# Optimization experiments

Hardware: AMD Instinct MI355X
Metric: run time of the kernel (lower is better)

Reference implementation:

```python
import jax, jax.numpy as jnp
import numpy as np
import math

H_SP, W_SP = 200, 200          # BEV spatial shape (single level, m == h)
D_MODEL = 256
N_HEADS = 8
N_POINTS = 4
D_HEAD = D_MODEL // N_HEADS


def _grid_init_bias():
    # Matches TemporalSelfAttention._reset_parameters for sampling_offsets.bias
    thetas = np.arange(N_HEADS, dtype=np.float32) * (2.0 * np.pi / N_HEADS)
    grid = np.stack([np.cos(thetas), np.sin(thetas)], -1)
    grid = grid / np.abs(grid).max(-1, keepdims=True)
    grid = np.tile(grid[:, None, None, :], (1, 1, N_POINTS, 1))  # (NH, 1, P, 2)
    for i in range(N_POINTS):
        grid[:, :, i, :] *= (i + 1)
    return jnp.asarray(grid.reshape(-1), dtype=jnp.float32)


def setup_inputs() -> dict:
    key = jax.random.key(0)
    ks = jax.random.split(key, 10)
    N = 1
    Lq = H_SP * W_SP
    Lin = H_SP * W_SP
    xav = math.sqrt(6.0 / (2 * D_MODEL))
    query = jax.random.normal(ks[0], (N, Lq, D_MODEL), jnp.float32)
    query_pos = jax.random.normal(ks[1], (N, Lq, D_MODEL), jnp.float32)
    reference_points = jax.random.uniform(ks[2], (N, Lq, 1, 2), jnp.float32)
    input_flatten = jax.random.normal(ks[3], (N, Lin, D_MODEL), jnp.float32)
    W_value = jax.random.uniform(ks[4], (D_MODEL, D_MODEL), jnp.float32, -xav, xav)
    b_value = jnp.zeros((D_MODEL,), jnp.float32)
    # small random weights (trained-model-like) + canonical grid bias
    W_off = jax.random.normal(ks[5], (N_HEADS * N_POINTS * 2, D_MODEL), jnp.float32) * 0.005
    b_off = _grid_init_bias()
    W_attn = jax.random.normal(ks[6], (N_HEADS * N_POINTS, D_MODEL), jnp.float32) * 0.02
    b_attn = jnp.zeros((N_HEADS * N_POINTS,), jnp.float32)
    W_out = jax.random.uniform(ks[7], (D_MODEL, D_MODEL), jnp.float32, -xav, xav)
    b_out = jnp.zeros((D_MODEL,), jnp.float32)
    return dict(query=query, query_pos=query_pos, reference_points=reference_points,
                input_flatten=input_flatten, W_value=W_value, b_value=b_value,
                W_off=W_off, b_off=b_off, W_attn=W_attn, b_attn=b_attn,
                W_out=W_out, b_out=b_out)


def _bilinear_sample(vflat, x, y):
    # vflat: (N, NH, H*W, DH); x, y: (N, NH, K) pixel coords (align_corners=False)
    # Zero padding outside the feature map, matching the MSDeformAttn CUDA kernel.
    x0f = jnp.floor(x)
    y0f = jnp.floor(y)
    x0 = x0f.astype(jnp.int32)
    y0 = y0f.astype(jnp.int32)
    lw = x - x0f
    lh = y - y0f
    gather = jax.vmap(jax.vmap(lambda v, i: v[i]))  # over batch, head
    acc = jnp.zeros(x.shape + (vflat.shape[-1],), vflat.dtype)
    corners = ((y0, x0, (1.0 - lh) * (1.0 - lw)),
               (y0, x0 + 1, (1.0 - lh) * lw),
               (y0 + 1, x0, lh * (1.0 - lw)),
               (y0 + 1, x0 + 1, lh * lw))
    for yi, xi, wgt in corners:
        valid = ((xi >= 0) & (xi < W_SP) & (yi >= 0) & (yi < H_SP)).astype(vflat.dtype)
        idx = jnp.clip(yi, 0, H_SP - 1) * W_SP + jnp.clip(xi, 0, W_SP - 1)
        g = gather(vflat, idx)                      # (N, NH, K, DH)
        acc = acc + (wgt * valid)[..., None] * g
    return acc


def reference(query, query_pos, reference_points, input_flatten,
              W_value, b_value, W_off, b_off, W_attn, b_attn, W_out, b_out):
    N, Lq, _ = query.shape
    q = query + query_pos
    value = input_flatten @ W_value.T + b_value                     # (N, Lin, D)
    value = value.reshape(N, -1, N_HEADS, D_HEAD).transpose(0, 2, 1, 3)  # (N, NH, Lin, DH)
    off = (q @ W_off.T + b_off).reshape(N, Lq, N_HEADS, N_POINTS, 2)
    attn = jax.nn.softmax((q @ W_attn.T + b_attn).reshape(N, Lq, N_HEADS, N_POINTS), axis=-1)
    norm = jnp.array([W_SP, H_SP], jnp.float32)                      # offset_normalizer (w, h)
    ref = reference_points[:, :, 0, :][:, :, None, None, :]          # (N, Lq, 1, 1, 2)
    loc = ref + off / norm                                           # (N, Lq, NH, P, 2) in [0,1]
    x = (loc[..., 0] * W_SP - 0.5).transpose(0, 2, 1, 3).reshape(N, N_HEADS, Lq * N_POINTS)
    y = (loc[..., 1] * H_SP - 0.5).transpose(0, 2, 1, 3).reshape(N, N_HEADS, Lq * N_POINTS)
    sampled = _bilinear_sample(value, x, y).reshape(N, N_HEADS, Lq, N_POINTS, D_HEAD)
    out = jnp.einsum('nhqpd,nqhp->nqhd', sampled, attn).reshape(N, Lq, D_MODEL)
    return out @ W_out.T + b_out
```

## Files before the change

### kernel.cpp

```cpp
#include <hip/hip_runtime.h>
#include <math.h>

#define LQ 40000
#define DMODEL 256
#define NHD 8
#define NPT 4
#define DHD 32
#define HSP 200
#define WSP 200

typedef short s16x8 __attribute__((ext_vector_type(8)));
typedef float f32x4 __attribute__((ext_vector_type(4)));

__device__ __forceinline__ unsigned short f2b(float f) {
    unsigned u = __builtin_bit_cast(unsigned, f);
    u += 0x7FFFu + ((u >> 16) & 1u);
    return (unsigned short)(u >> 16);
}
__device__ __forceinline__ float b2f(unsigned short u) {
    return __builtin_bit_cast(float, ((unsigned)u) << 16);
}
__device__ __forceinline__ void pk8(const float4& v0, const float4& v1,
                                    unsigned short* o) {
    o[0] = f2b(v0.x); o[1] = f2b(v0.y); o[2] = f2b(v0.z); o[3] = f2b(v0.w);
    o[4] = f2b(v1.x); o[5] = f2b(v1.y); o[6] = f2b(v1.z); o[7] = f2b(v1.w);
}


__global__ __launch_bounds__(256) void convert_weights(
    const float* __restrict__ Wv, const float* __restrict__ Woff,
    const float* __restrict__ Wattn, const float* __restrict__ Wout,
    unsigned short* __restrict__ dst)
{
    int u = blockIdx.x * 256 + threadIdx.x;
    int lane = u & 63, ks = (u >> 6) & 7, slot = u >> 9;
    int l15 = lane & 15, quad = lane >> 4;
    const float* src;
    if (slot < 16) {
        src = Wv + (size_t)(slot * 16 + l15) * 256;
    } else if (slot < 22) {
        int col = (slot - 16) * 16 + l15;
        src = (col < 64) ? Woff + (size_t)col * 256
                         : Wattn + (size_t)(col - 64) * 256;
    } else {
        src = Wout + (size_t)((slot - 22) * 16 + l15) * 256;
    }
    int k0 = ks * 32 + quad * 8;
    float4 v0 = *(const float4*)(src + k0);
    float4 v1 = *(const float4*)(src + k0 + 4);
    union { unsigned short u16[8]; uint4 v; } tmp;
    pk8(v0, v1, tmp.u16);
    *(uint4*)(dst + (size_t)u * 8) = tmp.v;
}

template <int NT, int TPW, int CMODE, bool HasA2>
__global__ __launch_bounds__(256, 2) void gemm_fused(
    const float* __restrict__ A, const float* __restrict__ A2,
    const unsigned short* __restrict__ Wf,
    const float* __restrict__ b1, const float* __restrict__ b2, int split,
    void* __restrict__ Cv)
{
    const int t = threadIdx.x;
    const int wave = t >> 6, lane = t & 63;
    const int l15 = lane & 15, quad = lane >> 4;

    s16x8 bf[TPW][8];
    float bias[TPW];
#pragma unroll
    for (int j = 0; j < TPW; ++j) {
        bias[j] = 0.f;
        int c = wave * TPW + j;
        if (c < NT) {
#pragma unroll
            for (int ks = 0; ks < 8; ++ks)
                bf[j][ks] = *(const s16x8*)&Wf[(size_t)(c * 8 + ks) * 512 + lane * 8];
            int col = c * 16 + l15;
            bias[j] = (col < split) ? b1[col] : b2[col - split];
        }
    }

#pragma unroll
    for (int s = 0; s < 2; ++s) {
        const size_t g = (size_t)blockIdx.x * 2 + s;
        const size_t rowoff = (g * 16 + l15) * 256;
        s16x8 a[8];
#pragma unroll
        for (int ks = 0; ks < 8; ++ks) {
            int k0 = ks * 32 + quad * 8;
            float4 v0 = *(const float4*)(A + rowoff + k0);
            float4 v1 = *(const float4*)(A + rowoff + k0 + 4);
            if constexpr (HasA2) {
                float4 w0 = *(const float4*)(A2 + rowoff + k0);
                float4 w1 = *(const float4*)(A2 + rowoff + k0 + 4);
                v0.x += w0.x; v0.y += w0.y; v0.z += w0.z; v0.w += w0.w;
                v1.x += w1.x; v1.y += w1.y; v1.z += w1.z; v1.w += w1.w;
            }
            union { unsigned short u16[8]; s16x8 v; } tmp;
            pk8(v0, v1, tmp.u16);
            a[ks] = tmp.v;
        }
#pragma unroll
        for (int j = 0; j < TPW; ++j) {
            int c = wave * TPW + j;
            if (c < NT) {
                f32x4 acc = (f32x4){0.f, 0.f, 0.f, 0.f};
#pragma unroll
                for (int ks = 0; ks < 8; ++ks)
                    acc = __builtin_amdgcn_mfma_f32_16x16x32_bf16(a[ks], bf[j][ks],
                                                                  acc, 0, 0, 0);
#pragma unroll
                for (int r2 = 0; r2 < 4; ++r2) {
                    size_t row = g * 16 + quad * 4 + r2;
                    float v = acc[r2] + bias[j];
                    if constexpr (CMODE == 1) {
                        ((unsigned short*)Cv)[(((size_t)(c >> 1) * LQ + row) << 5)
                                              + ((c & 1) << 4) + l15] = f2b(v);
                    } else if constexpr (CMODE == 2) {
                        int col = c * 16 + l15;
                        int hh, jj;
                        if (col < 64) { hh = col >> 3; jj = col & 7; }
                        else          { hh = (col - 64) >> 2; jj = 8 + (col & 3); }
                        ((float*)Cv)[((size_t)hh * LQ + row) * 12 + jj] = v;
                    } else {
                        ((float*)Cv)[row * (NT * 16) + c * 16 + l15] = v;
                    }
                }
            }
        }
    }
}

template <int NT, int TPW>
__global__ __launch_bounds__(256, 2) void gemm_rs(
    const unsigned short* __restrict__ Af, const unsigned short* __restrict__ Wf,
    const float* __restrict__ b1, float* __restrict__ C)
{
    const int t = threadIdx.x;
    const int wave = t >> 6, lane = t & 63;
    const int l15 = lane & 15, quad = lane >> 4;

    s16x8 bf[TPW][8];
    float bias[TPW];
#pragma unroll
    for (int j = 0; j < TPW; ++j) {
        int c = wave * TPW + j;
#pragma unroll
        for (int ks = 0; ks < 8; ++ks)
            bf[j][ks] = *(const s16x8*)&Wf[(size_t)(c * 8 + ks) * 512 + lane * 8];
        bias[j] = b1[c * 16 + l15];
    }

#pragma unroll
    for (int s = 0; s < 2; ++s) {
        const size_t g = (size_t)blockIdx.x * 2 + s;
        s16x8 a[8];
#pragma unroll
        for (int ks = 0; ks < 8; ++ks)
            a[ks] = *(const s16x8*)&Af[g * 4096 + ks * 512 + lane * 8];
#pragma unroll
        for (int j = 0; j < TPW; ++j) {
            int c = wave * TPW + j;
            f32x4 acc = (f32x4){0.f, 0.f, 0.f, 0.f};
#pragma unroll
            for (int ks = 0; ks < 8; ++ks)
                acc = __builtin_amdgcn_mfma_f32_16x16x32_bf16(a[ks], bf[j][ks],
                                                              acc, 0, 0, 0);
#pragma unroll
            for (int r2 = 0; r2 < 4; ++r2) {
                size_t row = g * 16 + quad * 4 + r2;
                C[row * (NT * 16) + c * 16 + l15] = acc[r2] + bias[j];
            }
        }
    }
}

__global__ __launch_bounds__(256) void sample_kernel(
    const float* __restrict__ raw2, const float* __restrict__ rp,
    const unsigned short* __restrict__ value, unsigned short* __restrict__ outa)
{
    __shared__ int4   sIdx[64][4];
    __shared__ float4 sW[64][4];

    const int h = blockIdx.x & 7;
    const int q0 = (blockIdx.x >> 3) * 64;
    const int t = threadIdx.x;
    {
        const int qi = t >> 2, p = t & 3;
        const int q = q0 + qi;
        const float* r = raw2 + ((size_t)h * LQ + q) * 12;
        float l0 = r[8], l1 = r[9], l2 = r[10], l3 = r[11];
        float mx = fmaxf(fmaxf(l0, l1), fmaxf(l2, l3));
        float e0 = __expf(l0 - mx), e1 = __expf(l1 - mx);
        float e2 = __expf(l2 - mx), e3 = __expf(l3 - mx);
        float inv = 1.f / (e0 + e1 + e2 + e3);
        float ep = (p == 0) ? e0 : (p == 1) ? e1 : (p == 2) ? e2 : e3;
        float wp = ep * inv;

        float x = rp[(size_t)q * 2 + 0] * (float)WSP - 0.5f + r[p * 2 + 0];
        float y = rp[(size_t)q * 2 + 1] * (float)HSP - 0.5f + r[p * 2 + 1];
        float x0f = floorf(x), y0f = floorf(y);
        int x0 = (int)x0f, y0 = (int)y0f;
        float lw = x - x0f, lh = y - y0f;
        float cw[4] = {(1.f - lh) * (1.f - lw), (1.f - lh) * lw,
                       lh * (1.f - lw), lh * lw};
        int4 I; float4 W;
        int* Ip = &I.x; float* Wp = &W.x;
#pragma unroll
        for (int c = 0; c < 4; ++c) {
            int cx = x0 + (c & 1), cy = y0 + (c >> 1);
            bool valid = (cx >= 0) & (cx < WSP) & (cy >= 0) & (cy < HSP);
            int ccx = cx < 0 ? 0 : (cx > WSP - 1 ? WSP - 1 : cx);
            int ccy = cy < 0 ? 0 : (cy > HSP - 1 ? HSP - 1 : cy);
            Ip[c] = (ccy * WSP + ccx) * DHD;
            Wp[c] = valid ? cw[c] * wp : 0.f;
        }
        sIdx[qi][p] = I;
        sW[qi][p] = W;
    }
    __syncthreads();

    const int d8 = t & 7, qp = t >> 3;
    const unsigned short* vp = value + (size_t)h * LQ * DHD + d8 * 4;
#pragma unroll
    for (int e = 0; e < 2; ++e) {
        int qi = qp * 2 + e;
        float a0 = 0.f, a1 = 0.f, a2 = 0.f, a3 = 0.f;
#pragma unroll
        for (int p = 0; p < 4; ++p) {
            int4 I = sIdx[qi][p];
            float4 W = sW[qi][p];
            uint2 g0 = *(const uint2*)(vp + I.x);
            uint2 g1 = *(const uint2*)(vp + I.y);
            uint2 g2 = *(const uint2*)(vp + I.z);
            uint2 g3 = *(const uint2*)(vp + I.w);
            a0 += W.x * b2f((unsigned short)g0.x);
            a1 += W.x * b2f((unsigned short)(g0.x >> 16));
            a2 += W.x * b2f((unsigned short)g0.y);
            a3 += W.x * b2f((unsigned short)(g0.y >> 16));
            a0 += W.y * b2f((unsigned short)g1.x);
            a1 += W.y * b2f((unsigned short)(g1.x >> 16));
            a2 += W.y * b2f((unsigned short)g1.y);
            a3 += W.y * b2f((unsigned short)(g1.y >> 16));
            a0 += W.z * b2f((unsigned short)g2.x);
            a1 += W.z * b2f((unsigned short)(g2.x >> 16));
            a2 += W.z * b2f((unsigned short)g2.y);
            a3 += W.z * b2f((unsigned short)(g2.y >> 16));
            a0 += W.w * b2f((unsigned short)g3.x);
            a1 += W.w * b2f((unsigned short)(g3.x >> 16));
            a2 += W.w * b2f((unsigned short)g3.y);
            a3 += W.w * b2f((unsigned short)(g3.y >> 16));
        }
        int q = q0 + qi;
        size_t off = (size_t)(q >> 4) * 4096 + h * 512 + (d8 >> 1) * 128
                   + (q & 15) * 8 + (d8 & 1) * 4;
        union { unsigned short u16[4]; uint2 v; } o;
        o.u16[0] = f2b(a0); o.u16[1] = f2b(a1);
        o.u16[2] = f2b(a2); o.u16[3] = f2b(a3);
        *(uint2*)&outa[off] = o.v;
    }
}

extern "C" void kernel_launch(void* const* d_in, const int* in_sizes, int n_in,
                              void* d_out, int out_size, void* d_ws, size_t ws_size,
                              hipStream_t stream)
{
    const float* query         = (const float*)d_in[0];
    const float* query_pos     = (const float*)d_in[1];
    const float* ref_points    = (const float*)d_in[2];
    const float* input_flatten = (const float*)d_in[3];
    const float* W_value       = (const float*)d_in[4];
    const float* b_value       = (const float*)d_in[5];
    const float* W_off         = (const float*)d_in[6];
    const float* b_off         = (const float*)d_in[7];
    const float* W_attn        = (const float*)d_in[8];
    const float* b_attn        = (const float*)d_in[9];
    const float* W_out         = (const float*)d_in[10];
    const float* b_out         = (const float*)d_in[11];
    float* out = (float*)d_out;

    unsigned short* val  = (unsigned short*)d_ws;
    float*          raw2 = (float*)(val + (size_t)LQ * DMODEL);
    unsigned short* outa = (unsigned short*)(raw2 + (size_t)LQ * 96);
    unsigned short* wf   = outa + (size_t)LQ * DMODEL;
    unsigned short* wfv  = wf;
    unsigned short* wfoa = wf + 65536;
    unsigned short* wfo  = wf + 90112;

    dim3 blk(256);

    convert_weights<<<dim3(76), blk, 0, stream>>>(W_value, W_off, W_attn, W_out, wf);

    gemm_fused<16, 4, 1, false><<<dim3(LQ / 32), blk, 0, stream>>>(
        input_flatten, nullptr, wfv, b_value, b_value, 256, val);

    gemm_fused<6, 2, 2, true><<<dim3(LQ / 32), blk, 0, stream>>>(
        query, query_pos, wfoa, b_off, b_attn, 64, raw2);

    sample_kernel<<<dim3(8 * (LQ / 64)), blk, 0, stream>>>(raw2, ref_points, val, outa);

    gemm_rs<16, 4><<<dim3(LQ / 32), blk, 0, stream>>>(outa, wfo, b_out, out);
}
```

Baseline: 259.7 us.

## Make GEMM kernels persistent with register-prefetched next strip

Turns the three GEMM kernels into persistent grid-stride loops over 16-row strips with a fixed grid of 512 blocks. Each iteration prefetches the next strip's A operand into registers before running the MFMAs on the current one, overlapping global loads with compute. Weight fragments are loaded once per block instead of once per two strips. In the value GEMM only half the weight tiles stay resident and the rest are reloaded each strip to limit register pressure. The extra prefetch registers may lower occupancy or cause spills.

```diff
diff --git a/kernel.cpp b/kernel.cpp
--- a/kernel.cpp
+++ b/kernel.cpp
@@ -8,6 +8,8 @@
 #define DHD 32
 #define HSP 200
 #define WSP 200
+#define NSTRIP (LQ / 16)
+#define GEMM_GRID 512
 
 typedef short s16x8 __attribute__((ext_vector_type(8)));
 typedef float f32x4 __attribute__((ext_vector_type(4)));
@@ -53,7 +55,7 @@
     *(uint4*)(dst + (size_t)u * 8) = tmp.v;
 }
 
-template <int NT, int TPW, int CMODE, bool HasA2>
+template <int NT, int TPW, int NBRES, int CMODE, bool HasA2>
 __global__ __launch_bounds__(256, 2) void gemm_fused(
     const float* __restrict__ A, const float* __restrict__ A2,
     const unsigned short* __restrict__ Wf,
@@ -64,53 +66,106 @@
     const int wave = t >> 6, lane = t & 63;
     const int l15 = lane & 15, quad = lane >> 4;
 
-    s16x8 bf[TPW][8];
+    s16x8 bf[NBRES][8];
     float bias[TPW];
 #pragma unroll
     for (int j = 0; j < TPW; ++j) {
         bias[j] = 0.f;
         int c = wave * TPW + j;
         if (c < NT) {
+            int col = c * 16 + l15;
+            bias[j] = (col < split) ? b1[col] : b2[col - split];
+        }
+    }
+#pragma unroll
+    for (int j = 0; j < NBRES; ++j) {
+        int c = wave * TPW + j;
+        if (c < NT) {
 #pragma unroll
             for (int ks = 0; ks < 8; ++ks)
                 bf[j][ks] = *(const s16x8*)&Wf[(size_t)(c * 8 + ks) * 512 + lane * 8];
-            int col = c * 16 + l15;
-            bias[j] = (col < split) ? b1[col] : b2[col - split];
-        }
-    }
-
-#pragma unroll
-    for (int s = 0; s < 2; ++s) {
-        const size_t g = (size_t)blockIdx.x * 2 + s;
-        const size_t rowoff = (g * 16 + l15) * 256;
+        }
+    }
+
+    float4 p0[8], p1[8], q0[8], q1[8];
+    s16x8 bs[TPW > NBRES ? (TPW - NBRES) : 1][8];
+
+    auto issue = [&](int gs) {
+        const float* base = A + ((size_t)gs * 16 + l15) * 256;
+#pragma unroll
+        for (int ks = 0; ks < 8; ++ks) {
+            const int k0 = ks * 32 + quad * 8;
+            p0[ks] = *(const float4*)(base + k0);
+            p1[ks] = *(const float4*)(base + k0 + 4);
+        }
+        if constexpr (HasA2) {
+            const float* base2 = A2 + ((size_t)gs * 16 + l15) * 256;
+#pragma unroll
+            for (int ks = 0; ks < 8; ++ks) {
+                const int k0 = ks * 32 + quad * 8;
+                q0[ks] = *(const float4*)(base2 + k0);
+                q1[ks] = *(const float4*)(base2 + k0 + 4);
+            }
+        }
+    };
+    auto issueB = [&]() {
+        if constexpr (TPW > NBRES) {
+#pragma unroll
+            for (int j = NBRES; j < TPW; ++j) {
+                int c = wave * TPW + j;
+                if (c < NT) {
+#pragma unroll
+                    for (int ks = 0; ks < 8; ++ks)
+                        bs[j - NBRES][ks] =
+                            *(const s16x8*)&Wf[(size_t)(c * 8 + ks) * 512 + lane * 8];
+                }
+            }
+        }
+    };
+
+    int g = blockIdx.x;
+    if (g < NSTRIP) { issue(g); issueB(); }
+    while (g < NSTRIP) {
         s16x8 a[8];
 #pragma unroll
         for (int ks = 0; ks < 8; ++ks) {
-            int k0 = ks * 32 + quad * 8;
-            float4 v0 = *(const float4*)(A + rowoff + k0);
-            float4 v1 = *(const float4*)(A + rowoff + k0 + 4);
+            float4 v0 = p0[ks], v1 = p1[ks];
             if constexpr (HasA2) {
-                float4 w0 = *(const float4*)(A2 + rowoff + k0);
-                float4 w1 = *(const float4*)(A2 + rowoff + k0 + 4);
-                v0.x += w0.x; v0.y += w0.y; v0.z += w0.z; v0.w += w0.w;
-                v1.x += w1.x; v1.y += w1.y; v1.z += w1.z; v1.w += w1.w;
+                v0.x += q0[ks].x; v0.y += q0[ks].y;
+                v0.z += q0[ks].z; v0.w += q0[ks].w;
+                v1.x += q1[ks].x; v1.y += q1[ks].y;
+                v1.z += q1[ks].z; v1.w += q1[ks].w;
             }
             union { unsigned short u16[8]; s16x8 v; } tmp;
             pk8(v0, v1, tmp.u16);
             a[ks] = tmp.v;
         }
+        s16x8 bcur[TPW > NBRES ? (TPW - NBRES) : 1][8];
+        if constexpr (TPW > NBRES) {
+#pragma unroll
+            for (int j = 0; j < TPW - NBRES; ++j)
+#pragma unroll
+                for (int ks = 0; ks < 8; ++ks) bcur[j][ks] = bs[j][ks];
+        }
+        const int gcur = g;
+        g += GEMM_GRID;
+        if (g < NSTRIP) { issue(g); issueB(); }
+
 #pragma unroll
         for (int j = 0; j < TPW; ++j) {
             int c = wave * TPW + j;
             if (c < NT) {
                 f32x4 acc = (f32x4){0.f, 0.f, 0.f, 0.f};
 #pragma unroll
-                for (int ks = 0; ks < 8; ++ks)
-                    acc = __builtin_amdgcn_mfma_f32_16x16x32_bf16(a[ks], bf[j][ks],
+                for (int ks = 0; ks < 8; ++ks) {
+                    s16x8 b = (j < NBRES) ? bf[j < NBRES ? j : 0][ks]
+                                          : bcur[j >= NBRES ? (j - NBRES) : 0][ks];
+                    acc = __builtin_amdgcn_mfma_f32_16x16x32_bf16(a[ks], b,
                                                                   acc, 0, 0, 0);
+                }
 #pragma unroll
                 for (int r2 = 0; r2 < 4; ++r2) {
-                    size_t row = g * 16 + quad * 4 + r2;
+                    size_t row = (size_t)gcur * 16 + quad * 4 + r2;
                     float v = acc[r2] + bias[j];
                     if constexpr (CMODE == 1) {
                         ((unsigned short*)Cv)[(((size_t)(c >> 1) * LQ + row) << 5)
@@ -150,13 +205,23 @@
         bias[j] = b1[c * 16 + l15];
     }
 
-#pragma unroll
-    for (int s = 0; s < 2; ++s) {
-        const size_t g = (size_t)blockIdx.x * 2 + s;
+    s16x8 p[8];
+    auto issue = [&](int gs) {
+#pragma unroll
+        for (int ks = 0; ks < 8; ++ks)
+            p[ks] = *(const s16x8*)&Af[(size_t)gs * 4096 + ks * 512 + lane * 8];
+    };
+
+    int g = blockIdx.x;
+    if (g < NSTRIP) issue(g);
+    while (g < NSTRIP) {
         s16x8 a[8];
 #pragma unroll
-        for (int ks = 0; ks < 8; ++ks)
-            a[ks] = *(const s16x8*)&Af[g * 4096 + ks * 512 + lane * 8];
+        for (int ks = 0; ks < 8; ++ks) a[ks] = p[ks];
+        const int gcur = g;
+        g += GEMM_GRID;
+        if (g < NSTRIP) issue(g);
+
 #pragma unroll
         for (int j = 0; j < TPW; ++j) {
             int c = wave * TPW + j;
@@ -167,7 +232,7 @@
                                                               acc, 0, 0, 0);
 #pragma unroll
             for (int r2 = 0; r2 < 4; ++r2) {
-                size_t row = g * 16 + quad * 4 + r2;
+                size_t row = (size_t)gcur * 16 + quad * 4 + r2;
                 C[row * (NT * 16) + c * 16 + l15] = acc[r2] + bias[j];
             }
         }
@@ -290,13 +355,13 @@
 
     convert_weights<<<dim3(76), blk, 0, stream>>>(W_value, W_off, W_attn, W_out, wf);
 
-    gemm_fused<16, 4, 1, false><<<dim3(LQ / 32), blk, 0, stream>>>(
+    gemm_fused<16, 4, 2, 1, false><<<dim3(GEMM_GRID), blk, 0, stream>>>(
         input_flatten, nullptr, wfv, b_value, b_value, 256, val);
 
-    gemm_fused<6, 2, 2, true><<<dim3(LQ / 32), blk, 0, stream>>>(
+    gemm_fused<6, 2, 2, 2, true><<<dim3(GEMM_GRID), blk, 0, stream>>>(
         query, query_pos, wfoa, b_off, b_attn, 64, raw2);
 
     sample_kernel<<<dim3(8 * (LQ / 64)), blk, 0, stream>>>(raw2, ref_points, val, outa);
 
-    gemm_rs<16, 4><<<dim3(LQ / 32), blk, 0, stream>>>(outa, wfo, b_out, out);
-}
+    gemm_rs<16, 4><<<dim3(GEMM_GRID), blk, 0, stream>>>(outa, wfo, b_out, out);
+}
```

Result: slower. 375.9 us (+44.8%).

## Make GEMM kernels persistent with LDS-staged, prefetched A tiles

Applied to the files above, without the earlier changes.

The three GEMM kernels now launch a fixed 512-block grid that strides over 16-row strips instead of one block per two strips. Each block loads the next strip's A rows into registers with coalesced float4/uint4 loads while computing the current strip from an LDS buffer. This removes the uncoalesced per-lane global A reads and amortises the weight-fragment register loads over more strips. In exchange it adds LDS use, two barriers per strip, and a lower block count that may leave latency less hidden.

```diff
diff --git a/kernel.cpp b/kernel.cpp
--- a/kernel.cpp
+++ b/kernel.cpp
@@ -8,6 +8,9 @@
 #define DHD 32
 #define HSP 200
 #define WSP 200
+#define NSTRIP (LQ / 16)
+#define GEMM_GRID 512
+#define RPAD 260
 
 typedef short s16x8 __attribute__((ext_vector_type(8)));
 typedef float f32x4 __attribute__((ext_vector_type(4)));
@@ -60,9 +63,13 @@
     const float* __restrict__ b1, const float* __restrict__ b2, int split,
     void* __restrict__ Cv)
 {
+    __shared__ float sbuf[HasA2 ? 2 : 1][16][RPAD];
+
     const int t = threadIdx.x;
     const int wave = t >> 6, lane = t & 63;
     const int l15 = lane & 15, quad = lane >> 4;
+    const int srow = t >> 4;
+    const int scol = (t & 15) * 4;
 
     s16x8 bf[TPW][8];
     float bias[TPW];
@@ -79,19 +86,41 @@
         }
     }
 
-#pragma unroll
-    for (int s = 0; s < 2; ++s) {
-        const size_t g = (size_t)blockIdx.x * 2 + s;
-        const size_t rowoff = (g * 16 + l15) * 256;
+    float4 r[HasA2 ? 8 : 4];
+    auto issue = [&](int gs) {
+        const float* base = A + ((size_t)gs * 16 + srow) * 256 + scol;
+#pragma unroll
+        for (int j = 0; j < 4; ++j) r[j] = *(const float4*)(base + j * 64);
+        if constexpr (HasA2) {
+            const float* base2 = A2 + ((size_t)gs * 16 + srow) * 256 + scol;
+#pragma unroll
+            for (int j = 0; j < 4; ++j) r[4 + j] = *(const float4*)(base2 + j * 64);
+        }
+    };
+
+    int g = blockIdx.x;
+    issue(g);
+    for (; g < NSTRIP; g += GEMM_GRID) {
+#pragma unroll
+        for (int j = 0; j < 4; ++j)
+            *(float4*)&sbuf[0][srow][scol + j * 64] = r[j];
+        if constexpr (HasA2) {
+#pragma unroll
+            for (int j = 0; j < 4; ++j)
+                *(float4*)&sbuf[1][srow][scol + j * 64] = r[4 + j];
+        }
+        __syncthreads();
+        if (g + GEMM_GRID < NSTRIP) issue(g + GEMM_GRID);
+
         s16x8 a[8];
 #pragma unroll
         for (int ks = 0; ks < 8; ++ks) {
-            int k0 = ks * 32 + quad * 8;
-            float4 v0 = *(const float4*)(A + rowoff + k0);
-            float4 v1 = *(const float4*)(A + rowoff + k0 + 4);
+            const int k0 = ks * 32 + quad * 8;
+            float4 v0 = *(const float4*)&sbuf[0][l15][k0];
+            float4 v1 = *(const float4*)&sbuf[0][l15][k0 + 4];
             if constexpr (HasA2) {
-                float4 w0 = *(const float4*)(A2 + rowoff + k0);
-                float4 w1 = *(const float4*)(A2 + rowoff + k0 + 4);
+                float4 w0 = *(const float4*)&sbuf[1][l15][k0];
+                float4 w1 = *(const float4*)&sbuf[1][l15][k0 + 4];
                 v0.x += w0.x; v0.y += w0.y; v0.z += w0.z; v0.w += w0.w;
                 v1.x += w1.x; v1.y += w1.y; v1.z += w1.z; v1.w += w1.w;
             }
@@ -99,6 +128,7 @@
             pk8(v0, v1, tmp.u16);
             a[ks] = tmp.v;
         }
+
 #pragma unroll
         for (int j = 0; j < TPW; ++j) {
             int c = wave * TPW + j;
@@ -110,7 +140,7 @@
                                                                   acc, 0, 0, 0);
 #pragma unroll
                 for (int r2 = 0; r2 < 4; ++r2) {
-                    size_t row = g * 16 + quad * 4 + r2;
+                    size_t row = (size_t)g * 16 + quad * 4 + r2;
                     float v = acc[r2] + bias[j];
                     if constexpr (CMODE == 1) {
                         ((unsigned short*)Cv)[(((size_t)(c >> 1) * LQ + row) << 5)
@@ -127,6 +157,7 @@
                 }
             }
         }
+        __syncthreads();
     }
 }
 
@@ -135,6 +166,8 @@
     const unsigned short* __restrict__ Af, const unsigned short* __restrict__ Wf,
     const float* __restrict__ b1, float* __restrict__ C)
 {
+    __shared__ unsigned short sbuf[4096];
+
     const int t = threadIdx.x;
     const int wave = t >> 6, lane = t & 63;
     const int l15 = lane & 15, quad = lane >> 4;
@@ -150,13 +183,26 @@
         bias[j] = b1[c * 16 + l15];
     }
 
-#pragma unroll
-    for (int s = 0; s < 2; ++s) {
-        const size_t g = (size_t)blockIdx.x * 2 + s;
+    uint4 r[2];
+    auto issue = [&](int gs) {
+        const char* base = (const char*)(Af + (size_t)gs * 4096) + t * 16;
+        r[0] = *(const uint4*)base;
+        r[1] = *(const uint4*)(base + 4096);
+    };
+
+    int g = blockIdx.x;
+    issue(g);
+    for (; g < NSTRIP; g += GEMM_GRID) {
+        *(uint4*)((char*)sbuf + t * 16) = r[0];
+        *(uint4*)((char*)sbuf + 4096 + t * 16) = r[1];
+        __syncthreads();
+        if (g + GEMM_GRID < NSTRIP) issue(g + GEMM_GRID);
+
         s16x8 a[8];
 #pragma unroll
         for (int ks = 0; ks < 8; ++ks)
-            a[ks] = *(const s16x8*)&Af[g * 4096 + ks * 512 + lane * 8];
+            a[ks] = *(const s16x8*)((const char*)sbuf + ks * 1024 + lane * 16);
+
 #pragma unroll
         for (int j = 0; j < TPW; ++j) {
             int c = wave * TPW + j;
@@ -167,10 +213,11 @@
                                                               acc, 0, 0, 0);
 #pragma unroll
             for (int r2 = 0; r2 < 4; ++r2) {
-                size_t row = g * 16 + quad * 4 + r2;
+                size_t row = (size_t)g * 16 + quad * 4 + r2;
                 C[row * (NT * 16) + c * 16 + l15] = acc[r2] + bias[j];
             }
         }
+        __syncthreads();
     }
 }
 
@@ -290,13 +337,13 @@
 
     convert_weights<<<dim3(76), blk, 0, stream>>>(W_value, W_off, W_attn, W_out, wf);
 
-    gemm_fused<16, 4, 1, false><<<dim3(LQ / 32), blk, 0, stream>>>(
+    gemm_fused<16, 4, 1, false><<<dim3(GEMM_GRID), blk, 0, stream>>>(
         input_flatten, nullptr, wfv, b_value, b_value, 256, val);
 
-    gemm_fused<6, 2, 2, true><<<dim3(LQ / 32), blk, 0, stream>>>(
+    gemm_fused<6, 2, 2, true><<<dim3(GEMM_GRID), blk, 0, stream>>>(
         query, query_pos, wfoa, b_off, b_attn, 64, raw2);
 
     sample_kernel<<<dim3(8 * (LQ / 64)), blk, 0, stream>>>(raw2, ref_points, val, outa);
 
-    gemm_rs<16, 4><<<dim3(LQ / 32), blk, 0, stream>>>(outa, wfo, b_out, out);
-}
+    gemm_rs<16, 4><<<dim3(GEMM_GRID), blk, 0, stream>>>(outa, wfo, b_out, out);
+}
```

After: 256.4 us. No clear change (-1.2%).

## Merge projection GEMMs into one launch and convert weights in-kernel

Applied to the files above, without the earlier changes.

Removes the separate weight-conversion kernel; each GEMM block now loads fp32 weights and packs them to bf16 itself. The value projection and the offset/attention projection now run as one launch with blocks split by index, cutting two launches. Activation loads are batched four k-slices at a time behind a compiler barrier to raise memory-level parallelism. Launch bounds drop to one block per CU. The cost is redundant per-block weight conversion, which adds global reads of fp32 weights (mostly served from cache) and extra convert work in every block.

```diff
diff --git a/kernel.cpp b/kernel.cpp
--- a/kernel.cpp
+++ b/kernel.cpp
@@ -27,38 +27,12 @@
 }
 
 
-__global__ __launch_bounds__(256) void convert_weights(
-    const float* __restrict__ Wv, const float* __restrict__ Woff,
-    const float* __restrict__ Wattn, const float* __restrict__ Wout,
-    unsigned short* __restrict__ dst)
-{
-    int u = blockIdx.x * 256 + threadIdx.x;
-    int lane = u & 63, ks = (u >> 6) & 7, slot = u >> 9;
-    int l15 = lane & 15, quad = lane >> 4;
-    const float* src;
-    if (slot < 16) {
-        src = Wv + (size_t)(slot * 16 + l15) * 256;
-    } else if (slot < 22) {
-        int col = (slot - 16) * 16 + l15;
-        src = (col < 64) ? Woff + (size_t)col * 256
-                         : Wattn + (size_t)(col - 64) * 256;
-    } else {
-        src = Wout + (size_t)((slot - 22) * 16 + l15) * 256;
-    }
-    int k0 = ks * 32 + quad * 8;
-    float4 v0 = *(const float4*)(src + k0);
-    float4 v1 = *(const float4*)(src + k0 + 4);
-    union { unsigned short u16[8]; uint4 v; } tmp;
-    pk8(v0, v1, tmp.u16);
-    *(uint4*)(dst + (size_t)u * 8) = tmp.v;
-}
-
 template <int NT, int TPW, int CMODE, bool HasA2>
-__global__ __launch_bounds__(256, 2) void gemm_fused(
-    const float* __restrict__ A, const float* __restrict__ A2,
-    const unsigned short* __restrict__ Wf,
-    const float* __restrict__ b1, const float* __restrict__ b2, int split,
-    void* __restrict__ Cv)
+__device__ __forceinline__ void gemm_body(
+    int g0, const float* __restrict__ A, const float* __restrict__ A2,
+    const float* __restrict__ W1, const float* __restrict__ W2,
+    const float* __restrict__ b1, const float* __restrict__ b2,
+    int split, void* __restrict__ Cv)
 {
     const int t = threadIdx.x;
     const int wave = t >> 6, lane = t & 63;
@@ -71,34 +45,60 @@
         bias[j] = 0.f;
         int c = wave * TPW + j;
         if (c < NT) {
-#pragma unroll
-            for (int ks = 0; ks < 8; ++ks)
-                bf[j][ks] = *(const s16x8*)&Wf[(size_t)(c * 8 + ks) * 512 + lane * 8];
-            int col = c * 16 + l15;
-            bias[j] = (col < split) ? b1[col] : b2[col - split];
+            int row = c * 16 + l15;
+            const float* ws = (row < split) ? W1 + (size_t)row * 256
+                                            : W2 + (size_t)(row - split) * 256;
+#pragma unroll
+            for (int ks = 0; ks < 8; ++ks) {
+                float4 v0 = *(const float4*)(ws + ks * 32 + quad * 8);
+                float4 v1 = *(const float4*)(ws + ks * 32 + quad * 8 + 4);
+                union { unsigned short u16[8]; s16x8 v; } tmp;
+                pk8(v0, v1, tmp.u16);
+                bf[j][ks] = tmp.v;
+            }
+            bias[j] = (row < split) ? b1[row] : b2[row - split];
         }
     }
 
 #pragma unroll
     for (int s = 0; s < 2; ++s) {
-        const size_t g = (size_t)blockIdx.x * 2 + s;
-        const size_t rowoff = (g * 16 + l15) * 256;
+        const size_t g = (size_t)g0 * 2 + s;
+        const float* base = A + (g * 16 + l15) * 256;
         s16x8 a[8];
 #pragma unroll
-        for (int ks = 0; ks < 8; ++ks) {
-            int k0 = ks * 32 + quad * 8;
-            float4 v0 = *(const float4*)(A + rowoff + k0);
-            float4 v1 = *(const float4*)(A + rowoff + k0 + 4);
+        for (int h = 0; h < 2; ++h) {
+            float4 p0[4], p1[4], q0[4], q1[4];
+#pragma unroll
+            for (int i = 0; i < 4; ++i) {
+                const int k0 = (h * 4 + i) * 32 + quad * 8;
+                p0[i] = *(const float4*)(base + k0);
+                p1[i] = *(const float4*)(base + k0 + 4);
+            }
             if constexpr (HasA2) {
-                float4 w0 = *(const float4*)(A2 + rowoff + k0);
-                float4 w1 = *(const float4*)(A2 + rowoff + k0 + 4);
-                v0.x += w0.x; v0.y += w0.y; v0.z += w0.z; v0.w += w0.w;
-                v1.x += w1.x; v1.y += w1.y; v1.z += w1.z; v1.w += w1.w;
-            }
-            union { unsigned short u16[8]; s16x8 v; } tmp;
-            pk8(v0, v1, tmp.u16);
-            a[ks] = tmp.v;
-        }
+                const float* base2 = A2 + (g * 16 + l15) * 256;
+#pragma unroll
+                for (int i = 0; i < 4; ++i) {
+                    const int k0 = (h * 4 + i) * 32 + quad * 8;
+                    q0[i] = *(const float4*)(base2 + k0);
+                    q1[i] = *(const float4*)(base2 + k0 + 4);
+                }
+            }
+            asm volatile("" ::: "memory");
+#pragma unroll
+            for (int i = 0; i < 4; ++i) {
+                float4 v0 = p0[i], v1 = p1[i];
+                if constexpr (HasA2) {
+                    v0.x += q0[i].x; v0.y += q0[i].y;
+                    v0.z += q0[i].z; v0.w += q0[i].w;
+                    v1.x += q1[i].x; v1.y += q1[i].y;
+                    v1.z += q1[i].z; v1.w += q1[i].w;
+                }
+                union { unsigned short u16[8]; s16x8 v; } tmp;
+                pk8(v0, v1, tmp.u16);
+                a[h * 4 + i] = tmp.v;
+            }
+        }
+
 #pragma unroll
         for (int j = 0; j < TPW; ++j) {
             int c = wave * TPW + j;
@@ -130,24 +130,47 @@
     }
 }
 
-template <int NT, int TPW>
-__global__ __launch_bounds__(256, 2) void gemm_rs(
-    const unsigned short* __restrict__ Af, const unsigned short* __restrict__ Wf,
-    const float* __restrict__ b1, float* __restrict__ C)
+__global__ __launch_bounds__(256, 1) void gemm12(
+    const float* __restrict__ input_flatten,
+    const float* __restrict__ query, const float* __restrict__ query_pos,
+    const float* __restrict__ Wv,   const float* __restrict__ bv,
+    const float* __restrict__ Woff, const float* __restrict__ boff,
+    const float* __restrict__ Wattn,const float* __restrict__ battn,
+    unsigned short* __restrict__ val, float* __restrict__ raw2)
+{
+    const int bid = blockIdx.x;
+    if (bid < LQ / 32) {
+        gemm_body<16, 4, 1, false>(bid, input_flatten, nullptr,
+                                   Wv, Wv, bv, bv, 256, val);
+    } else {
+        gemm_body<6, 2, 2, true>(bid - LQ / 32, query, query_pos,
+                                 Woff, Wattn, boff, battn, 64, raw2);
+    }
+}
+
+__global__ __launch_bounds__(256, 1) void gemm4(
+    const unsigned short* __restrict__ Af, const float* __restrict__ Wout,
+    const float* __restrict__ bout, float* __restrict__ C)
 {
     const int t = threadIdx.x;
     const int wave = t >> 6, lane = t & 63;
     const int l15 = lane & 15, quad = lane >> 4;
 
-    s16x8 bf[TPW][8];
-    float bias[TPW];
-#pragma unroll
-    for (int j = 0; j < TPW; ++j) {
-        int c = wave * TPW + j;
-#pragma unroll
-        for (int ks = 0; ks < 8; ++ks)
-            bf[j][ks] = *(const s16x8*)&Wf[(size_t)(c * 8 + ks) * 512 + lane * 8];
-        bias[j] = b1[c * 16 + l15];
+    s16x8 bf[4][8];
+    float bias[4];
+#pragma unroll
+    for (int j = 0; j < 4; ++j) {
+        int c = wave * 4 + j;
+        const float* ws = Wout + (size_t)(c * 16 + l15) * 256;
+#pragma unroll
+        for (int ks = 0; ks < 8; ++ks) {
+            float4 v0 = *(const float4*)(ws + ks * 32 + quad * 8);
+            float4 v1 = *(const float4*)(ws + ks * 32 + quad * 8 + 4);
+            union { unsigned short u16[8]; s16x8 v; } tmp;
+            pk8(v0, v1, tmp.u16);
+            bf[j][ks] = tmp.v;
+        }
+        bias[j] = bout[c * 16 + l15];
     }
 
 #pragma unroll
@@ -157,9 +180,10 @@
 #pragma unroll
         for (int ks = 0; ks < 8; ++ks)
             a[ks] = *(const s16x8*)&Af[g * 4096 + ks * 512 + lane * 8];
-#pragma unroll
-        for (int j = 0; j < TPW; ++j) {
-            int c = wave * TPW + j;
+        asm volatile("" ::: "memory");
+#pragma unroll
+        for (int j = 0; j < 4; ++j) {
+            int c = wave * 4 + j;
             f32x4 acc = (f32x4){0.f, 0.f, 0.f, 0.f};
 #pragma unroll
             for (int ks = 0; ks < 8; ++ks)
@@ -168,7 +192,7 @@
 #pragma unroll
             for (int r2 = 0; r2 < 4; ++r2) {
                 size_t row = g * 16 + quad * 4 + r2;
-                C[row * (NT * 16) + c * 16 + l15] = acc[r2] + bias[j];
+                C[row * 256 + c * 16 + l15] = acc[r2] + bias[j];
             }
         }
     }
@@ -281,22 +305,14 @@
     unsigned short* val  = (unsigned short*)d_ws;
     float*          raw2 = (float*)(val + (size_t)LQ * DMODEL);
     unsigned short* outa = (unsigned short*)(raw2 + (size_t)LQ * 96);
-    unsigned short* wf   = outa + (size_t)LQ * DMODEL;
-    unsigned short* wfv  = wf;
-    unsigned short* wfoa = wf + 65536;
-    unsigned short* wfo  = wf + 90112;
 
     dim3 blk(256);
 
-    convert_weights<<<dim3(76), blk, 0, stream>>>(W_value, W_off, W_attn, W_out, wf);
-
-    gemm_fused<16, 4, 1, false><<<dim3(LQ / 32), blk, 0, stream>>>(
-        input_flatten, nullptr, wfv, b_value, b_value, 256, val);
-
-    gemm_fused<6, 2, 2, true><<<dim3(LQ / 32), blk, 0, stream>>>(
-        query, query_pos, wfoa, b_off, b_attn, 64, raw2);
+    gemm12<<<dim3(2 * (LQ / 32)), blk, 0, stream>>>(
+        input_flatten, query, query_pos,
+        W_value, b_value, W_off, b_off, W_attn, b_attn, val, raw2);
 
     sample_kernel<<<dim3(8 * (LQ / 64)), blk, 0, stream>>>(raw2, ref_points, val, outa);
 
-    gemm_rs<16, 4><<<dim3(LQ / 32), blk, 0, stream>>>(outa, wfo, b_out, out);
-}
+    gemm4<<<dim3(LQ / 32), blk, 0, stream>>>(outa, W_out, b_out, out);
+}
```

Result: slower. 314.7 us (+21.2%).
